# Optimization experiments

Hardware: AMD Instinct MI355X
Metric: run time of the kernel (lower is better)

## Reference

```python
import jax, jax.numpy as jnp
import numpy as np

N_EMB = 1024
HEAD_SIZE = 64
BLOCK_SIZE = 2048
B, T = 8, 2048


def setup_inputs() -> dict:
    key = jax.random.key(0)
    kx, kq, kk, kv = jax.random.split(key, 4)
    scale = 1.0 / (N_EMB ** 0.5)
    x = jax.random.normal(kx, (B, T, N_EMB), dtype=jnp.float32)
    Wq = jax.random.uniform(kq, (N_EMB, HEAD_SIZE), dtype=jnp.float32) * scale
    Wk = jax.random.uniform(kk, (N_EMB, HEAD_SIZE), dtype=jnp.float32) * scale
    Wv = jax.random.uniform(kv, (N_EMB, HEAD_SIZE), dtype=jnp.float32) * scale
    return {"x": x, "Wq": Wq, "Wk": Wk, "Wv": Wv}


def reference(x, Wq, Wk, Wv):
    # Faithful to Head.__call__ with is_training=False.
    # NOTE: original code applies NO 1/sqrt(head_size) scaling to the scores.
    Bt, Tt, _ = x.shape
    q = x @ Wq                      # (B, T, H)
    k = x @ Wk                      # (B, T, H)
    v = x @ Wv                      # (B, T, H)
    wei = jnp.einsum('bth,bsh->bts', q, k)  # (B, T, T)
    causal = jnp.tril(jnp.ones((Tt, Tt), dtype=bool))
    wei = jnp.where(causal, wei, -jnp.inf)
    wei = jax.nn.softmax(wei, axis=-1)
    out = jnp.einsum('bts,bsh->bth', wei, v)  # (B, T, H)
    return out
```

## Files before the change

kernel.cpp:

```cpp
#include <hip/hip_runtime.h>
#include <hip/hip_bf16.h>

#define BB 8
#define TT 2048
#define EE 1024
#define HH 64

typedef __attribute__((ext_vector_type(8))) short short8;
typedef __attribute__((ext_vector_type(4))) float f32x4;

__device__ inline f32x4 mfma_16x16x32(short8 a, short8 b, f32x4 c) {
  return __builtin_amdgcn_mfma_f32_16x16x32_bf16(a, b, c, 0, 0, 0);
}

__device__ inline void gload_lds16(const __hip_bfloat16* g, __hip_bfloat16* l) {
  __builtin_amdgcn_global_load_lds((const __attribute__((address_space(1))) void*)g,
                                   (__attribute__((address_space(3))) void*)l,
                                   16, 0, 0);
}

__device__ inline short f2bf(float f) {
  __hip_bfloat16 h = __float2bfloat16(f);
  return *reinterpret_cast<short*>(&h);
}
__device__ inline float bf2f(short s) {
  __hip_bfloat16 h = *reinterpret_cast<__hip_bfloat16*>(&s);
  return __bfloat162float(h);
}

#define WAIT_LGKM0() __builtin_amdgcn_s_waitcnt(0xC07F)

__global__ void prep_w(const float* __restrict__ Wq, const float* __restrict__ Wk,
                       const float* __restrict__ Wv,
                       __hip_bfloat16* __restrict__ Wthi,
                       __hip_bfloat16* __restrict__ Wtlo,
                       float* __restrict__ maxk2) {
  const int n = blockIdx.x;
  if (n == 0 && threadIdx.x < 8) maxk2[threadIdx.x] = 0.f;
  const int m = n >> 6;
  const int h = n & 63;
  const float* W = (m == 0) ? Wq : (m == 1) ? Wk : Wv;
  const int e0 = threadIdx.x * 4;
#pragma unroll
  for (int j = 0; j < 4; ++j) {
    const float w = W[(e0 + j) * 64 + h];
    const __hip_bfloat16 hi = __float2bfloat16(w);
    Wthi[n * 1024 + e0 + j] = hi;
    Wtlo[n * 1024 + e0 + j] = __float2bfloat16(w - __bfloat162float(hi));
  }
}

__global__ __launch_bounds__(256) void qkv_gemm(
    const float* __restrict__ x,
    const __hip_bfloat16* __restrict__ Wthi, const __hip_bfloat16* __restrict__ Wtlo,
    __hip_bfloat16* __restrict__ qhi, __hip_bfloat16* __restrict__ qlo,
    __hip_bfloat16* __restrict__ khi, __hip_bfloat16* __restrict__ klo,
    __hip_bfloat16* __restrict__ vT) {
  __shared__ __hip_bfloat16 Ahi[2][32 * 72];
  __shared__ __hip_bfloat16 Alo[2][32 * 72];
  __shared__ __hip_bfloat16 Bhi[2][192 * 64];

  const int tid  = threadIdx.x;
  const int wave = tid >> 6;
  const int lane = tid & 63;
  const int row0 = blockIdx.x * 32;
  const int l15 = lane & 15, l4 = lane >> 4;

  const int lr = tid >> 3;
  const int le = (tid & 7) * 8;
  const float* xrow = x + (row0 + lr) * 1024 + le;

  f32x4 acc[2][3];
#pragma unroll
  for (int m = 0; m < 2; ++m)
#pragma unroll
    for (int j = 0; j < 3; ++j) acc[m][j] = f32x4{0.f, 0.f, 0.f, 0.f};

  auto issue_Bhi = [&](int c, int buf) {
    const int g = (lane & 7) ^ ((lane >> 3) & 7);
#pragma unroll
    for (int s = 0; s < 3; ++s) {
      const int j = wave + s * 4;
#pragma unroll
      for (int qh = 0; qh < 2; ++qh) {
        const int qq = j * 2 + qh;
        const int n  = qq * 8 + (lane >> 3);
        gload_lds16(Wthi + n * 1024 + c * 64 + g * 8, &Bhi[buf][qq * 512]);
      }
    }
  };
  auto load_Blo = [&](int c, short8* bl) {
#pragma unroll
    for (int jj = 0; jj < 2; ++jj) {
      const int j = wave + jj * 4;
      const __hip_bfloat16* p = Wtlo + (j * 16 + l15) * 1024 + c * 64;
      bl[jj * 2]     = *(const short8*)(p + l4 * 8);
      bl[jj * 2 + 1] = *(const short8*)(p + 32 + l4 * 8);
    }
  };
  auto write_A = [&](int buf, const f32x4* xr) {
    short8 h0, l0;
    const float* xf = (const float*)xr;
#pragma unroll
    for (int j = 0; j < 8; ++j) {
      const float v = xf[j];
      const short h = f2bf(v);
      h0[j] = h;
      l0[j] = f2bf(v - bf2f(h));
    }
    *(short8*)&Ahi[buf][lr * 72 + le] = h0;
    *(short8*)&Alo[buf][lr * 72 + le] = l0;
  };
  auto compute = [&](int buf, const short8* bl) {
#pragma unroll
    for (int m = 0; m < 2; ++m) {
      const int tr = m * 16 + l15;
      short8 ah0 = *(const short8*)&Ahi[buf][tr * 72 + l4 * 8];
      short8 ah1 = *(const short8*)&Ahi[buf][tr * 72 + 32 + l4 * 8];
      short8 al0 = *(const short8*)&Alo[buf][tr * 72 + l4 * 8];
      short8 al1 = *(const short8*)&Alo[buf][tr * 72 + 32 + l4 * 8];
#pragma unroll
      for (int jj = 0; jj < 3; ++jj) {
        const int j  = (jj < 2) ? (wave + jj * 4) : (wave + 8);
        const int n  = j * 16 + l15;
        const int o0 = ((l4)     ^ (n & 7)) * 8;
        const int o1 = ((4 + l4) ^ (n & 7)) * 8;
        short8 bh0 = *(const short8*)&Bhi[buf][n * 64 + o0];
        short8 bh1 = *(const short8*)&Bhi[buf][n * 64 + o1];
        acc[m][jj] = mfma_16x16x32(ah0, bh0, acc[m][jj]);
        acc[m][jj] = mfma_16x16x32(ah1, bh1, acc[m][jj]);
        if (jj < 2) {
          acc[m][jj] = mfma_16x16x32(ah0, bl[jj * 2],     acc[m][jj]);
          acc[m][jj] = mfma_16x16x32(ah1, bl[jj * 2 + 1], acc[m][jj]);
          acc[m][jj] = mfma_16x16x32(al0, bh0, acc[m][jj]);
          acc[m][jj] = mfma_16x16x32(al1, bh1, acc[m][jj]);
        }
      }
    }
  };

  f32x4 xr[2], xn[2];
  {
    const f32x4* p = (const f32x4*)xrow;
    xr[0] = p[0]; xr[1] = p[1];
  }
  short8 blc[4], bln[4];
  issue_Bhi(0, 0);
  load_Blo(0, blc);
  __builtin_amdgcn_s_waitcnt(0);
  write_A(0, xr);
  __syncthreads();

  for (int c = 0; c < 16; ++c) {
    const int p = c & 1;
    if (c < 15) {
      const f32x4* pp = (const f32x4*)(xrow + (c + 1) * 64);
      xn[0] = pp[0]; xn[1] = pp[1];
      issue_Bhi(c + 1, p ^ 1);
      load_Blo(c + 1, bln);
    }
    compute(p, blc);
    if (c < 15) {
      __builtin_amdgcn_s_waitcnt(0);
      write_A(p ^ 1, xn);
#pragma unroll
      for (int q = 0; q < 4; ++q) blc[q] = bln[q];
    }
    __syncthreads();
  }

  const int hcol = wave * 16 + l15;
#pragma unroll
  for (int jj = 0; jj < 3; ++jj) {
#pragma unroll
    for (int m = 0; m < 2; ++m) {
#pragma unroll
      for (int r = 0; r < 4; ++r) {
        const int trow = row0 + m * 16 + l4 * 4 + r;
        const float val = acc[m][jj][r];
        if (jj == 0) {
          const __hip_bfloat16 hi = __float2bfloat16(val);
          qhi[trow * 64 + hcol] = hi;
          qlo[trow * 64 + hcol] = __float2bfloat16(val - __bfloat162float(hi));
        } else if (jj == 1) {
          const __hip_bfloat16 hi = __float2bfloat16(val);
          khi[trow * 64 + hcol] = hi;
          klo[trow * 64 + hcol] = __float2bfloat16(val - __bfloat162float(hi));
        } else {
          const int bb = trow >> 11, tl = trow & 2047;
          vT[(bb * 64 + hcol) * 2048 + tl] = __float2bfloat16(val);
        }
      }
    }
  }
}

__global__ __launch_bounds__(256) void knorm(
    const __hip_bfloat16* __restrict__ khi, const __hip_bfloat16* __restrict__ klo,
    float* __restrict__ maxk2) {
  const int row = blockIdx.x * 256 + threadIdx.x;
  const int b = row >> 11;
  const __hip_bfloat16* ph = khi + row * 64;
  const __hip_bfloat16* pl = klo + row * 64;
  float s = 0.f;
#pragma unroll
  for (int i = 0; i < 8; ++i) {
    const short8 h = *(const short8*)(ph + i * 8);
    const short8 l = *(const short8*)(pl + i * 8);
#pragma unroll
    for (int j = 0; j < 8; ++j) {
      const float v = bf2f(h[j]) + bf2f(l[j]);
      s += v * v;
    }
  }
  for (int off = 1; off < 64; off <<= 1) s = fmaxf(s, __shfl_xor(s, off));
  if ((threadIdx.x & 63) == 0)
    atomicMax((int*)&maxk2[b], __float_as_int(s));
}

__global__ __launch_bounds__(256, 2) void attn(
    const __hip_bfloat16* __restrict__ qhi, const __hip_bfloat16* __restrict__ qlo,
    const __hip_bfloat16* __restrict__ khi, const __hip_bfloat16* __restrict__ klo,
    const __hip_bfloat16* __restrict__ vT, const float* __restrict__ maxk2,
    float* __restrict__ out) {
  __shared__ __hip_bfloat16 Psm[4][16 * 72];
  __shared__ float Osm[4][16][65];
  __shared__ float Lsm[4][16];

  const int tid  = threadIdx.x;
  const int wave = tid >> 6;
  const int lane = tid & 63;
  const int l15 = lane & 15, l4 = lane >> 4;

  const int b  = blockIdx.x & 7;
  const int ss = 127 - (blockIdx.x >> 3);
  const int t0 = ss * 16;
  const int ntiles = (ss >> 2) + 1;

  const __hip_bfloat16* qph = qhi + (b * 2048 + t0 + l15) * 64;
  const __hip_bfloat16* qpl = qlo + (b * 2048 + t0 + l15) * 64;
  const short8 qh0 = *(const short8*)(qph + l4 * 8);
  const short8 qh1 = *(const short8*)(qph + 32 + l4 * 8);
  const short8 ql0 = *(const short8*)(qpl + l4 * 8);
  const short8 ql1 = *(const short8*)(qpl + 32 + l4 * 8);

  float qn = 0.f;
#pragma unroll
  for (int i = 0; i < 8; ++i) {
    const float v0 = bf2f(qh0[i]) + bf2f(ql0[i]);
    const float v1 = bf2f(qh1[i]) + bf2f(ql1[i]);
    qn += v0 * v0 + v1 * v1;
  }
  qn += __shfl_xor(qn, 16);
  qn += __shfl_xor(qn, 32);
  const float kmax = sqrtf(maxk2[b]);
  const float crow = sqrtf(qn) * kmax + 2.0f;
  float c_[4];
#pragma unroll
  for (int r = 0; r < 4; ++r) c_[r] = __shfl(crow, l4 * 4 + r);

  short8 ones;
#pragma unroll
  for (int i = 0; i < 8; ++i) ones[i] = (short)0x3F80;

  f32x4 acc[4];
#pragma unroll
  for (int j = 0; j < 4; ++j) acc[j] = f32x4{0.f, 0.f, 0.f, 0.f};
  f32x4 accL = f32x4{0.f, 0.f, 0.f, 0.f};

  const __hip_bfloat16* kbase_h = khi + (size_t)b * 2048 * 64;
  const __hip_bfloat16* kbase_l = klo + (size_t)b * 2048 * 64;
  const __hip_bfloat16* vbase   = vT + (size_t)b * 64 * 2048;

  for (int kt = wave; kt < ntiles; kt += 4) {
    const int k0 = kt << 6;
    const bool diag = (kt == ntiles - 1);

    f32x4 s_[4];
#pragma unroll
    for (int st = 0; st < 2; ++st) {
      short8 kh0[2], kh1[2], kl0[2], kl1[2];
#pragma unroll
      for (int jj = 0; jj < 2; ++jj) {
        const int j = st * 2 + jj;
        if (!(diag && (k0 + j * 16) > (t0 + 15))) {
          const __hip_bfloat16* kph = kbase_h + (k0 + j * 16 + l15) * 64;
          const __hip_bfloat16* kpl = kbase_l + (k0 + j * 16 + l15) * 64;
          kh0[jj] = *(const short8*)(kph + l4 * 8);
          kh1[jj] = *(const short8*)(kph + 32 + l4 * 8);
          kl0[jj] = *(const short8*)(kpl + l4 * 8);
          kl1[jj] = *(const short8*)(kpl + 32 + l4 * 8);
        }
      }
#pragma unroll
      for (int jj = 0; jj < 2; ++jj) {
        const int j = st * 2 + jj;
        if (diag && (k0 + j * 16) > (t0 + 15)) {
          s_[j] = f32x4{-1e30f, -1e30f, -1e30f, -1e30f};
        } else {
          f32x4 z = f32x4{0.f, 0.f, 0.f, 0.f};
          z = mfma_16x16x32(qh0, kh0[jj], z);
          z = mfma_16x16x32(qh1, kh1[jj], z);
          z = mfma_16x16x32(qh0, kl0[jj], z);
          z = mfma_16x16x32(qh1, kl1[jj], z);
          z = mfma_16x16x32(ql0, kh0[jj], z);
          z = mfma_16x16x32(ql1, kh1[jj], z);
          s_[j] = z;
        }
      }
    }

    if (diag) {
#pragma unroll
      for (int j = 0; j < 4; ++j) {
        const int key = k0 + j * 16 + l15;
#pragma unroll
        for (int r = 0; r < 4; ++r) {
          const int row = t0 + l4 * 4 + r;
          if (key > row) s_[j][r] = -1e30f;
        }
      }
    }

#pragma unroll
    for (int j = 0; j < 4; ++j)
#pragma unroll
      for (int r = 0; r < 4; ++r) s_[j][r] = __expf(s_[j][r] - c_[r]);

#pragma unroll
    for (int j = 0; j < 4; ++j)
#pragma unroll
      for (int r = 0; r < 4; ++r)
        Psm[wave][(l4 * 4 + r) * 72 + j * 16 + l15] = __float2bfloat16(s_[j][r]);

    short8 vf0[4], vf1[4];
#pragma unroll
    for (int j = 0; j < 4; ++j) {
      const __hip_bfloat16* vp = vbase + (j * 16 + l15) * 2048 + k0;
      vf0[j] = *(const short8*)(vp + l4 * 8);
      vf1[j] = *(const short8*)(vp + 32 + l4 * 8);
    }

    WAIT_LGKM0();

    const short8 pf0 = *(const short8*)&Psm[wave][l15 * 72 + l4 * 8];
    const short8 pf1 = *(const short8*)&Psm[wave][l15 * 72 + 32 + l4 * 8];
#pragma unroll
    for (int j = 0; j < 4; ++j) {
      acc[j] = mfma_16x16x32(pf0, vf0[j], acc[j]);
      acc[j] = mfma_16x16x32(pf1, vf1[j], acc[j]);
    }
    accL = mfma_16x16x32(pf0, ones, accL);
    accL = mfma_16x16x32(pf1, ones, accL);
  }

#pragma unroll
  for (int j = 0; j < 4; ++j)
#pragma unroll
    for (int r = 0; r < 4; ++r)
      Osm[wave][l4 * 4 + r][j * 16 + l15] = acc[j][r];
  if (l15 == 0) {
#pragma unroll
    for (int r = 0; r < 4; ++r) Lsm[wave][l4 * 4 + r] = accL[r];
  }
  __syncthreads();

#pragma unroll
  for (int rr = 0; rr < 4; ++rr) {
    const int row = wave * 4 + rr;
    const float L = Lsm[0][row] + Lsm[1][row] + Lsm[2][row] + Lsm[3][row];
    float O = Osm[0][row][lane] + Osm[1][row][lane] +
              Osm[2][row][lane] + Osm[3][row][lane];
    out[(b * 2048 + t0 + row) * 64 + lane] = O / L;
  }
}

extern "C" void kernel_launch(void* const* d_in, const int* in_sizes, int n_in,
                              void* d_out, int out_size, void* d_ws, size_t ws_size,
                              hipStream_t stream) {
  const float* x  = (const float*)d_in[0];
  const float* Wq = (const float*)d_in[1];
  const float* Wk = (const float*)d_in[2];
  const float* Wv = (const float*)d_in[3];
  float* out = (float*)d_out;

  char* ws = (char*)d_ws;
  __hip_bfloat16* Wthi = (__hip_bfloat16*)ws;
  __hip_bfloat16* Wtlo = (__hip_bfloat16*)(ws + 393216);
  __hip_bfloat16* qhi  = (__hip_bfloat16*)(ws + 786432);
  __hip_bfloat16* qlo  = (__hip_bfloat16*)(ws + 786432 + 1 * 2097152);
  __hip_bfloat16* khi  = (__hip_bfloat16*)(ws + 786432 + 2 * 2097152);
  __hip_bfloat16* klo  = (__hip_bfloat16*)(ws + 786432 + 3 * 2097152);
  __hip_bfloat16* vT   = (__hip_bfloat16*)(ws + 786432 + 4 * 2097152);
  float* maxk2         = (float*)(ws + 786432 + 5 * 2097152);

  prep_w<<<192, 256, 0, stream>>>(Wq, Wk, Wv, Wthi, Wtlo, maxk2);
  qkv_gemm<<<512, 256, 0, stream>>>(x, Wthi, Wtlo, qhi, qlo, khi, klo, vT);
  knorm<<<64, 256, 0, stream>>>(khi, klo, maxk2);
  attn<<<1024, 256, 0, stream>>>(qhi, qlo, khi, klo, vT, maxk2, out);
}
```

Before: 184.9 us.

## Process 32 query rows per block and prefetch next K tile into registers

Each attention block now handles two 16-row query sub-tiles, 32 rows in all, so each loaded K and V tile is reused across both. The grid is halved to 512 blocks and the block order is interleaved, heavy then light, to balance causal work. K for the next tile is prefetched into registers while the current tile's softmax and PV run. This adds register pressure from doubled Q, K and accumulator state, which may reduce occupancy, and halves the number of blocks available to spread across CUs.

```diff
diff --git a/kernel.cpp b/kernel.cpp
--- a/kernel.cpp
+++ b/kernel.cpp
@@ -223,115 +223,123 @@
     const __hip_bfloat16* __restrict__ khi, const __hip_bfloat16* __restrict__ klo,
     const __hip_bfloat16* __restrict__ vT, const float* __restrict__ maxk2,
     float* __restrict__ out) {
-  __shared__ __hip_bfloat16 Psm[4][16 * 72];
-  __shared__ float Osm[4][16][65];
-  __shared__ float Lsm[4][16];
+  __shared__ __hip_bfloat16 Psm[4][2][16 * 72];
+  __shared__ float Osm[4][32][65];
+  __shared__ float Lsm[4][32];
 
   const int tid  = threadIdx.x;
   const int wave = tid >> 6;
   const int lane = tid & 63;
   const int l15 = lane & 15, l4 = lane >> 4;
 
-  const int b  = blockIdx.x & 7;
-  const int ss = 127 - (blockIdx.x >> 3);
-  const int t0 = ss * 16;
-  const int ntiles = (ss >> 2) + 1;
-
-  const __hip_bfloat16* qph = qhi + (b * 2048 + t0 + l15) * 64;
-  const __hip_bfloat16* qpl = qlo + (b * 2048 + t0 + l15) * 64;
-  const short8 qh0 = *(const short8*)(qph + l4 * 8);
-  const short8 qh1 = *(const short8*)(qph + 32 + l4 * 8);
-  const short8 ql0 = *(const short8*)(qpl + l4 * 8);
-  const short8 ql1 = *(const short8*)(qpl + 32 + l4 * 8);
-
-  float qn = 0.f;
-#pragma unroll
-  for (int i = 0; i < 8; ++i) {
-    const float v0 = bf2f(qh0[i]) + bf2f(ql0[i]);
-    const float v1 = bf2f(qh1[i]) + bf2f(ql1[i]);
-    qn += v0 * v0 + v1 * v1;
-  }
-  qn += __shfl_xor(qn, 16);
-  qn += __shfl_xor(qn, 32);
+  const int b = blockIdx.x & 7;
+  const int g = blockIdx.x >> 3;
+  const int ss = (g < 32) ? (63 - g) : (g - 32);
+  const int t0 = ss * 32;
+  const int ntiles = (ss >> 1) + 1;
+
+  short8 qh0[2], qh1[2], ql0[2], ql1[2];
+#pragma unroll
+  for (int m = 0; m < 2; ++m) {
+    const __hip_bfloat16* qph = qhi + (b * 2048 + t0 + m * 16 + l15) * 64;
+    const __hip_bfloat16* qpl = qlo + (b * 2048 + t0 + m * 16 + l15) * 64;
+    qh0[m] = *(const short8*)(qph + l4 * 8);
+    qh1[m] = *(const short8*)(qph + 32 + l4 * 8);
+    ql0[m] = *(const short8*)(qpl + l4 * 8);
+    ql1[m] = *(const short8*)(qpl + 32 + l4 * 8);
+  }
+
   const float kmax = sqrtf(maxk2[b]);
-  const float crow = sqrtf(qn) * kmax + 2.0f;
-  float c_[4];
-#pragma unroll
-  for (int r = 0; r < 4; ++r) c_[r] = __shfl(crow, l4 * 4 + r);
+  float c_[2][4];
+#pragma unroll
+  for (int m = 0; m < 2; ++m) {
+    float qn = 0.f;
+#pragma unroll
+    for (int i = 0; i < 8; ++i) {
+      const float v0 = bf2f(qh0[m][i]) + bf2f(ql0[m][i]);
+      const float v1 = bf2f(qh1[m][i]) + bf2f(ql1[m][i]);
+      qn += v0 * v0 + v1 * v1;
+    }
+    qn += __shfl_xor(qn, 16);
+    qn += __shfl_xor(qn, 32);
+    const float crow = sqrtf(qn) * kmax + 2.0f;
+#pragma unroll
+    for (int r = 0; r < 4; ++r) c_[m][r] = __shfl(crow, l4 * 4 + r);
+  }
 
   short8 ones;
 #pragma unroll
   for (int i = 0; i < 8; ++i) ones[i] = (short)0x3F80;
 
-  f32x4 acc[4];
-#pragma unroll
-  for (int j = 0; j < 4; ++j) acc[j] = f32x4{0.f, 0.f, 0.f, 0.f};
-  f32x4 accL = f32x4{0.f, 0.f, 0.f, 0.f};
+  f32x4 acc[2][4];
+#pragma unroll
+  for (int m = 0; m < 2; ++m)
+#pragma unroll
+    for (int j = 0; j < 4; ++j) acc[m][j] = f32x4{0.f, 0.f, 0.f, 0.f};
+  f32x4 accL[2];
+  accL[0] = f32x4{0.f, 0.f, 0.f, 0.f};
+  accL[1] = f32x4{0.f, 0.f, 0.f, 0.f};
 
   const __hip_bfloat16* kbase_h = khi + (size_t)b * 2048 * 64;
   const __hip_bfloat16* kbase_l = klo + (size_t)b * 2048 * 64;
   const __hip_bfloat16* vbase   = vT + (size_t)b * 64 * 2048;
 
+  short8 kh0[4], kh1[4], kl0[4], kl1[4];
+  auto load_K = [&](int k0) {
+#pragma unroll
+    for (int j = 0; j < 4; ++j) {
+      const __hip_bfloat16* kph = kbase_h + (k0 + j * 16 + l15) * 64;
+      const __hip_bfloat16* kpl = kbase_l + (k0 + j * 16 + l15) * 64;
+      kh0[j] = *(const short8*)(kph + l4 * 8);
+      kh1[j] = *(const short8*)(kph + 32 + l4 * 8);
+      kl0[j] = *(const short8*)(kpl + l4 * 8);
+      kl1[j] = *(const short8*)(kpl + 32 + l4 * 8);
+    }
+  };
+
+  if (wave < ntiles) load_K(wave << 6);
+
   for (int kt = wave; kt < ntiles; kt += 4) {
     const int k0 = kt << 6;
     const bool diag = (kt == ntiles - 1);
 
     f32x4 s_[4];
 #pragma unroll
-    for (int st = 0; st < 2; ++st) {
-      short8 kh0[2], kh1[2], kl0[2], kl1[2];
-#pragma unroll
-      for (int jj = 0; jj < 2; ++jj) {
-        const int j = st * 2 + jj;
-        if (!(diag && (k0 + j * 16) > (t0 + 15))) {
-          const __hip_bfloat16* kph = kbase_h + (k0 + j * 16 + l15) * 64;
-          const __hip_bfloat16* kpl = kbase_l + (k0 + j * 16 + l15) * 64;
-          kh0[jj] = *(const short8*)(kph + l4 * 8);
-          kh1[jj] = *(const short8*)(kph + 32 + l4 * 8);
-          kl0[jj] = *(const short8*)(kpl + l4 * 8);
-          kl1[jj] = *(const short8*)(kpl + 32 + l4 * 8);
-        }
-      }
-#pragma unroll
-      for (int jj = 0; jj < 2; ++jj) {
-        const int j = st * 2 + jj;
-        if (diag && (k0 + j * 16) > (t0 + 15)) {
+    for (int m = 0; m < 2; ++m) {
+      const int rowmax = t0 + m * 16 + 15;
+#pragma unroll
+      for (int j = 0; j < 4; ++j) {
+        if (diag && (k0 + j * 16) > rowmax) {
           s_[j] = f32x4{-1e30f, -1e30f, -1e30f, -1e30f};
         } else {
           f32x4 z = f32x4{0.f, 0.f, 0.f, 0.f};
-          z = mfma_16x16x32(qh0, kh0[jj], z);
-          z = mfma_16x16x32(qh1, kh1[jj], z);
-          z = mfma_16x16x32(qh0, kl0[jj], z);
-          z = mfma_16x16x32(qh1, kl1[jj], z);
-          z = mfma_16x16x32(ql0, kh0[jj], z);
-          z = mfma_16x16x32(ql1, kh1[jj], z);
+          z = mfma_16x16x32(qh0[m], kh0[j], z);
+          z = mfma_16x16x32(qh1[m], kh1[j], z);
+          z = mfma_16x16x32(qh0[m], kl0[j], z);
+          z = mfma_16x16x32(qh1[m], kl1[j], z);
+          z = mfma_16x16x32(ql0[m], kh0[j], z);
+          z = mfma_16x16x32(ql1[m], kh1[j], z);
           s_[j] = z;
         }
       }
-    }
-
-    if (diag) {
-#pragma unroll
-      for (int j = 0; j < 4; ++j) {
-        const int key = k0 + j * 16 + l15;
+      if (m == 1) break;
+      if (diag) {
+#pragma unroll
+        for (int j = 0; j < 4; ++j) {
+          const int key = k0 + j * 16 + l15;
+#pragma unroll
+          for (int r = 0; r < 4; ++r)
+            if (key > (t0 + l4 * 4 + r)) s_[j][r] = -1e30f;
+        }
+      }
+#pragma unroll
+      for (int j = 0; j < 4; ++j)
 #pragma unroll
         for (int r = 0; r < 4; ++r) {
-          const int row = t0 + l4 * 4 + r;
-          if (key > row) s_[j][r] = -1e30f;
+          const float pv = __expf(s_[j][r] - c_[0][r]);
+          Psm[wave][0][(l4 * 4 + r) * 72 + j * 16 + l15] = __float2bfloat16(pv);
         }
-      }
-    }
-
-#pragma unroll
-    for (int j = 0; j < 4; ++j)
-#pragma unroll
-      for (int r = 0; r < 4; ++r) s_[j][r] = __expf(s_[j][r] - c_[r]);
-
-#pragma unroll
-    for (int j = 0; j < 4; ++j)
-#pragma unroll
-      for (int r = 0; r < 4; ++r)
-        Psm[wave][(l4 * 4 + r) * 72 + j * 16 + l15] = __float2bfloat16(s_[j][r]);
+    }
 
     short8 vf0[4], vf1[4];
 #pragma unroll
@@ -340,37 +348,62 @@
       vf0[j] = *(const short8*)(vp + l4 * 8);
       vf1[j] = *(const short8*)(vp + 32 + l4 * 8);
     }
+    if (kt + 4 < ntiles) load_K((kt + 4) << 6);
+
+    if (diag) {
+#pragma unroll
+      for (int j = 0; j < 4; ++j) {
+        const int key = k0 + j * 16 + l15;
+#pragma unroll
+        for (int r = 0; r < 4; ++r)
+          if (key > (t0 + 16 + l4 * 4 + r)) s_[j][r] = -1e30f;
+      }
+    }
+#pragma unroll
+    for (int j = 0; j < 4; ++j)
+#pragma unroll
+      for (int r = 0; r < 4; ++r) {
+        const float pv = __expf(s_[j][r] - c_[1][r]);
+        Psm[wave][1][(l4 * 4 + r) * 72 + j * 16 + l15] = __float2bfloat16(pv);
+      }
 
     WAIT_LGKM0();
 
-    const short8 pf0 = *(const short8*)&Psm[wave][l15 * 72 + l4 * 8];
-    const short8 pf1 = *(const short8*)&Psm[wave][l15 * 72 + 32 + l4 * 8];
-#pragma unroll
-    for (int j = 0; j < 4; ++j) {
-      acc[j] = mfma_16x16x32(pf0, vf0[j], acc[j]);
-      acc[j] = mfma_16x16x32(pf1, vf1[j], acc[j]);
-    }
-    accL = mfma_16x16x32(pf0, ones, accL);
-    accL = mfma_16x16x32(pf1, ones, accL);
-  }
-
-#pragma unroll
-  for (int j = 0; j < 4; ++j)
-#pragma unroll
-    for (int r = 0; r < 4; ++r)
-      Osm[wave][l4 * 4 + r][j * 16 + l15] = acc[j][r];
-  if (l15 == 0) {
-#pragma unroll
-    for (int r = 0; r < 4; ++r) Lsm[wave][l4 * 4 + r] = accL[r];
+#pragma unroll
+    for (int m = 0; m < 2; ++m) {
+      const short8 pf0 = *(const short8*)&Psm[wave][m][l15 * 72 + l4 * 8];
+      const short8 pf1 = *(const short8*)&Psm[wave][m][l15 * 72 + 32 + l4 * 8];
+#pragma unroll
+      for (int j = 0; j < 4; ++j) {
+        acc[m][j] = mfma_16x16x32(pf0, vf0[j], acc[m][j]);
+        acc[m][j] = mfma_16x16x32(pf1, vf1[j], acc[m][j]);
+      }
+      accL[m] = mfma_16x16x32(pf0, ones, accL[m]);
+      accL[m] = mfma_16x16x32(pf1, ones, accL[m]);
+    }
+  }
+
+#pragma unroll
+  for (int m = 0; m < 2; ++m) {
+#pragma unroll
+    for (int j = 0; j < 4; ++j)
+#pragma unroll
+      for (int r = 0; r < 4; ++r)
+        Osm[wave][m * 16 + l4 * 4 + r][j * 16 + l15] = acc[m][j][r];
+    if (l15 == 0) {
+#pragma unroll
+      for (int r = 0; r < 4; ++r)
+        Lsm[wave][m * 16 + l4 * 4 + r] = accL[m][r];
+    }
   }
   __syncthreads();
 
 #pragma unroll
-  for (int rr = 0; rr < 4; ++rr) {
-    const int row = wave * 4 + rr;
+  for (int rr = 0; rr < 8; ++rr) {
+    const int row = wave * 8 + rr;
     const float L = Lsm[0][row] + Lsm[1][row] + Lsm[2][row] + Lsm[3][row];
-    float O = Osm[0][row][lane] + Osm[1][row][lane] +
-              Osm[2][row][lane] + Osm[3][row][lane];
+    const float O = Osm[0][row][lane] + Osm[1][row][lane] +
+                    Osm[2][row][lane] + Osm[3][row][lane];
     out[(b * 2048 + t0 + row) * 64 + lane] = O / L;
   }
 }
@@ -397,5 +430,5 @@
   prep_w<<<192, 256, 0, stream>>>(Wq, Wk, Wv, Wthi, Wtlo, maxk2);
   qkv_gemm<<<512, 256, 0, stream>>>(x, Wthi, Wtlo, qhi, qlo, khi, klo, vT);
   knorm<<<64, 256, 0, stream>>>(khi, klo, maxk2);
-  attn<<<1024, 256, 0, stream>>>(qhi, qlo, khi, klo, vT, maxk2, out);
-}
+  attn<<<512, 256, 0, stream>>>(qhi, qlo, khi, klo, vT, maxk2, out);
+}
```

After: 162.6 us. -12.1%, faster.
